# Performance work log

Measured on AMD Instinct MI355X. Metric: run time of the kernel, lower is better.

The kernel has to match this reference:

```python
import jax, jax.numpy as jnp
import numpy as np

MARGIN = 0.5
AP_VALUE = 0.8
AN_VALUE = 0.4
ABS_W = 1.0


def setup_inputs() -> dict:
    key = jax.random.key(0)
    k1, k2 = jax.random.split(key)
    bs, d = 16384, 64
    inputs = jax.random.normal(k1, (bs, d), dtype=jnp.float32)
    target = jax.random.randint(k2, (bs,), 0, 64, dtype=jnp.int64)
    return {"inputs": inputs, "target": target}


def reference(inputs, target):
    # L2-normalize features (normalize_feature=True)
    x = inputs / jnp.linalg.norm(inputs, axis=-1, keepdims=True)

    # cross-entropy on normalized features treated as logits
    logp = jax.nn.log_softmax(x, axis=-1)  # [bs, d]
    loss_ce = -jnp.mean(jnp.take_along_axis(logp, target[:, None], axis=1))

    # cosine-similarity matrix [bs, bs]
    dist = x @ x.T

    is_pos = target[None, :] == target[:, None]
    # hard mining: min similarity among positives, max among negatives (per row)
    dist_ap = jnp.min(jnp.where(is_pos, dist, jnp.inf), axis=1)   # [bs]
    dist_an = jnp.max(jnp.where(is_pos, -jnp.inf, dist), axis=1)  # [bs]

    loss = jnp.mean(jax.nn.relu(MARGIN + dist_ap - dist_an))

    # absolute (angular margin) terms
    abs_ap = jax.nn.relu(AP_VALUE - dist_ap)
    abs_an = jax.nn.relu(dist_an - AN_VALUE)
    loss = (jnp.mean(abs_an) + jnp.mean(abs_ap)) * ABS_W + loss

    return loss + loss_ce
```

## Files before the change

### kernel.cpp

```cpp
#include <hip/hip_runtime.h>


#define N_ROWS 16384
#define N_DIM 64

typedef __attribute__((ext_vector_type(8))) short bf16x8;
typedef __attribute__((ext_vector_type(4))) float f32x4;

__device__ inline unsigned short f2bf(float f) {
  unsigned u = __float_as_uint(f);
  unsigned r = u + 0x7fffu + ((u >> 16) & 1u);
  return (unsigned short)(r >> 16);
}

__device__ inline unsigned enc_key(float f) {
  unsigned u = __float_as_uint(f);
  return (u & 0x80000000u) ? ~u : (u | 0x80000000u);
}
__device__ inline float dec_key(unsigned k) {
  unsigned u = (k & 0x80000000u) ? (k ^ 0x80000000u) : ~k;
  return __uint_as_float(u);
}

__device__ inline void g2lds16(const void* g, void* l) {
  __builtin_amdgcn_global_load_lds(
      (const __attribute__((address_space(1))) void*)g,
      (__attribute__((address_space(3))) void*)l, 16, 0, 0);
}

__global__ void prep_kernel(const float* __restrict__ x, const int* __restrict__ tgt,
                            unsigned short* __restrict__ xb, float* __restrict__ ce_row,
                            unsigned* __restrict__ mp_key, unsigned* __restrict__ mn_key,
                            float* __restrict__ out) {
  const int row  = blockIdx.x * 4 + (threadIdx.x >> 6);
  const int lane = threadIdx.x & 63;
  float v  = x[row * N_DIM + lane];
  float ss = v * v;
#pragma unroll
  for (int s = 1; s < 64; s <<= 1) ss += __shfl_xor(ss, s, 64);
  float xn = v * rsqrtf(ss);
  xb[row * N_DIM + lane] = f2bf(xn);

  float mx = xn;
#pragma unroll
  for (int s = 1; s < 64; s <<= 1) mx = fmaxf(mx, __shfl_xor(mx, s, 64));
  float e  = __expf(xn - mx);
  float se = e;
#pragma unroll
  for (int s = 1; s < 64; s <<= 1) se += __shfl_xor(se, s, 64);
  float lse = mx + __logf(se);
  int   t   = tgt[row];
  float xt  = __shfl(xn, t, 64);
  if (lane == 0) {
    ce_row[row] = lse - xt;
    mp_key[row] = 0xFFFFFFFFu;
    mn_key[row] = 0u;
  }
  if (blockIdx.x == 0 && threadIdx.x == 0) out[0] = 0.f;
}

__global__ __launch_bounds__(256, 8)
void mine_kernel(const unsigned short* __restrict__ xb, const int* __restrict__ tgt,
                 unsigned* __restrict__ mp_key, unsigned* __restrict__ mn_key) {
  __shared__ unsigned short Bt[2][4][1024];
  __shared__ unsigned short tjl[N_ROWS / 16];

  const int lane    = threadIdx.x & 63;
  const int wv      = threadIdx.x >> 6;
  const int iblk    = blockIdx.x >> 4;
  const int jspl    = blockIdx.x & 15;
  const int rowbase = iblk * 128 + wv * 32;
  const int m = lane & 15, q = lane >> 4;
  const int jbase = jspl * (N_ROWS / 16);

  bf16x8 a[2][2];
#pragma unroll
  for (int tr = 0; tr < 2; ++tr) {
    const unsigned short* p = xb + (rowbase + tr * 16 + m) * N_DIM + q * 8;
    a[tr][0] = *(const bf16x8*)(p);
    a[tr][1] = *(const bf16x8*)(p + 32);
  }
  int ti[2][4];
#pragma unroll
  for (int tr = 0; tr < 2; ++tr)
#pragma unroll
    for (int r = 0; r < 4; ++r)
      ti[tr][r] = tgt[rowbase + tr * 16 + q * 4 + r];

  float mp[8], mn[8];
#pragma unroll
  for (int k = 0; k < 8; ++k) { mp[k] = __builtin_inff(); mn[k] = -__builtin_inff(); }

  for (int k = threadIdx.x; k < N_ROWS / 16; k += 256)
    tjl[k] = (unsigned short)tgt[jbase + k];

  const unsigned short* src0 =
      xb + (jbase + (lane >> 3)) * N_DIM + (((lane & 7) ^ ((lane >> 3) & 7)) * 8);

#define STAGE(P, BUF)                                                            \
  do {                                                                           \
    const unsigned short* s_ = src0 + ((P) * 64 + wv * 16) * N_DIM;              \
    g2lds16(s_,             (unsigned short*)&Bt[(BUF)][wv][0] + lane * 8);      \
    g2lds16(s_ + 8 * N_DIM, (unsigned short*)&Bt[(BUF)][wv][0] + 512 + lane * 8);\
  } while (0)

  STAGE(0, 0);
  STAGE(1, 1);
  __syncthreads();

  const int roff0 = m * 128 + ((q * 16) ^ ((m & 7) << 4));
  const int roff1 = m * 128 + (((64) + q * 16) ^ ((m & 7) << 4));

  for (int ph = 0; ph < 16; ++ph) {
    const int pb = ph & 1;
#pragma unroll 1
    for (int j4 = 0; j4 < 4; ++j4) {
      const int jc = ph * 4 + j4;
      const char* bb = (const char*)&Bt[pb][j4][0];
      const bf16x8 cb0 = *(const bf16x8*)(bb + roff0);
      const bf16x8 cb1 = *(const bf16x8*)(bb + roff1);
      const int    ctj = tjl[jc * 16 + m];

#pragma unroll
      for (int tr = 0; tr < 2; ++tr) {
        f32x4 acc = {0.f, 0.f, 0.f, 0.f};
        acc = __builtin_amdgcn_mfma_f32_16x16x32_bf16(a[tr][0], cb0, acc, 0, 0, 0);
        acc = __builtin_amdgcn_mfma_f32_16x16x32_bf16(a[tr][1], cb1, acc, 0, 0, 0);
#pragma unroll
        for (int r = 0; r < 4; ++r) {
          const bool  pos = (ctj == ti[tr][r]);
          const float d   = acc[r];
          const int   k   = tr * 4 + r;
          mp[k] = fminf(mp[k], pos ? d : __builtin_inff());
          mn[k] = fmaxf(mn[k], pos ? -__builtin_inff() : d);
        }
      }
    }
    __builtin_amdgcn_s_barrier();
    if (ph < 14) {
      STAGE(ph + 2, pb);
      asm volatile("s_waitcnt vmcnt(2)" ::: "memory");
      __builtin_amdgcn_sched_barrier(0);
      __builtin_amdgcn_s_barrier();
    } else if (ph == 14) {
      asm volatile("s_waitcnt vmcnt(0)" ::: "memory");
      __builtin_amdgcn_sched_barrier(0);
      __builtin_amdgcn_s_barrier();
    }
  }

#pragma unroll
  for (int s = 1; s < 16; s <<= 1) {
#pragma unroll
    for (int k = 0; k < 8; ++k) {
      mp[k] = fminf(mp[k], __shfl_xor(mp[k], s, 64));
      mn[k] = fmaxf(mn[k], __shfl_xor(mn[k], s, 64));
    }
  }
  if (m == 0) {
#pragma unroll
    for (int tr = 0; tr < 2; ++tr)
#pragma unroll
      for (int r = 0; r < 4; ++r) {
        const int row = rowbase + tr * 16 + q * 4 + r;
        atomicMin(&mp_key[row], enc_key(mp[tr * 4 + r]));
        atomicMax(&mn_key[row], enc_key(mn[tr * 4 + r]));
      }
  }
#undef STAGE
}

__global__ void finalize_kernel(const unsigned* __restrict__ mp_key, const unsigned* __restrict__ mn_key,
                                const float* __restrict__ ce_row, float* __restrict__ out) {
  __shared__ float red[16];
  float s = 0.f;
#pragma unroll
  for (int it = 0; it < 2; ++it) {
    const int r = it * 8192 + blockIdx.x * 1024 + threadIdx.x;
    float ap = dec_key(mp_key[r]);
    float an = dec_key(mn_key[r]);
    s += fmaxf(0.5f + ap - an, 0.f) + fmaxf(0.8f - ap, 0.f) +
         fmaxf(an - 0.4f, 0.f) + ce_row[r];
  }
#pragma unroll
  for (int sh = 1; sh < 64; sh <<= 1) s += __shfl_xor(s, sh, 64);
  const int wv = threadIdx.x >> 6;
  if ((threadIdx.x & 63) == 0) red[wv] = s;
  __syncthreads();
  if (threadIdx.x == 0) {
    float t = 0.f;
#pragma unroll
    for (int w = 0; w < 16; ++w) t += red[w];
    atomicAdd(out, t * (1.0f / N_ROWS));
  }
}

extern "C" void kernel_launch(void* const* d_in, const int* in_sizes, int n_in,
                              void* d_out, int out_size, void* d_ws, size_t ws_size,
                              hipStream_t stream) {
  const float* x   = (const float*)d_in[0];
  const int*   tgt = (const int*)d_in[1];
  char* ws = (char*)d_ws;

  unsigned short* xb     = (unsigned short*)ws;
  unsigned*       mp_key = (unsigned*)(ws + (2u << 20));
  unsigned*       mn_key = (unsigned*)(ws + (2u << 20) + (64u << 10));
  float*          ce_row = (float*)(ws + (2u << 20) + (128u << 10));
  float*          out    = (float*)d_out;

  prep_kernel<<<N_ROWS / 4, 256, 0, stream>>>(x, tgt, xb, ce_row, mp_key, mn_key, out);
  mine_kernel<<<(N_ROWS / 128) * 16, 256, 0, stream>>>(xb, tgt, mp_key, mn_key);
  finalize_kernel<<<8, 1024, 0, stream>>>(mp_key, mn_key, ce_row, out);
}
```

Measured before the change: 157.3 us.

## Software-pipeline MFMA and mining across column tiles, simplify LDS staging

Unrolls the per-phase column-tile loop and software-pipelines it so the MFMAs for the next 16-column tile are issued before the min/max mining of the previous tile's results, overlapping matrix-core latency with VALU work. LDS staging moves from a prefetch-two-ahead scheme with explicit vmcnt waits and double barriers to a prefetch-one-ahead issue at the top of each phase followed by a single __syncthreads. Launch bounds drop from 8 to 6 waves per SIMD to leave room for the extra live accumulators. The shallower prefetch and lower occupancy may expose more load latency.

Measured after the change: 199.6 us. 1.27x slower.

```diff
diff --git a/kernel.cpp b/kernel.cpp
--- a/kernel.cpp
+++ b/kernel.cpp
@@ -59,7 +59,7 @@
   if (blockIdx.x == 0 && threadIdx.x == 0) out[0] = 0.f;
 }
 
-__global__ __launch_bounds__(256, 8)
+__global__ __launch_bounds__(256, 6)
 void mine_kernel(const unsigned short* __restrict__ xb, const int* __restrict__ tgt,
                  unsigned* __restrict__ mp_key, unsigned* __restrict__ mn_key) {
   __shared__ unsigned short Bt[2][4][1024];
@@ -97,57 +97,74 @@
   const unsigned short* src0 =
       xb + (jbase + (lane >> 3)) * N_DIM + (((lane & 7) ^ ((lane >> 3) & 7)) * 8);
 
-#define STAGE(P, BUF)                                                            \
-  do {                                                                           \
-    const unsigned short* s_ = src0 + ((P) * 64 + wv * 16) * N_DIM;              \
+#define STAGE(P_, BUF)                                                           \
+  do {                                                                           \
+    const unsigned short* s_ = src0 + ((P_) * 64 + wv * 16) * N_DIM;             \
     g2lds16(s_,             (unsigned short*)&Bt[(BUF)][wv][0] + lane * 8);      \
     g2lds16(s_ + 8 * N_DIM, (unsigned short*)&Bt[(BUF)][wv][0] + 512 + lane * 8);\
   } while (0)
 
   STAGE(0, 0);
-  STAGE(1, 1);
   __syncthreads();
 
   const int roff0 = m * 128 + ((q * 16) ^ ((m & 7) << 4));
   const int roff1 = m * 128 + (((64) + q * 16) ^ ((m & 7) << 4));
 
+#define MFMA_JC(D0, D1, CB0, CB1)                                                \
+  do {                                                                           \
+    const f32x4 z_ = {0.f, 0.f, 0.f, 0.f};                                       \
+    D0 = __builtin_amdgcn_mfma_f32_16x16x32_bf16(a[0][0], CB0, z_, 0, 0, 0);     \
+    D0 = __builtin_amdgcn_mfma_f32_16x16x32_bf16(a[0][1], CB1, D0, 0, 0, 0);     \
+    D1 = __builtin_amdgcn_mfma_f32_16x16x32_bf16(a[1][0], CB0, z_, 0, 0, 0);     \
+    D1 = __builtin_amdgcn_mfma_f32_16x16x32_bf16(a[1][1], CB1, D1, 0, 0, 0);     \
+  } while (0)
+
+#define JC_STEP(J4, D0, D1, CTV)                                                 \
+  do {                                                                           \
+    const bf16x8 cb0_ = *(const bf16x8*)(bb + (J4) * 2048 + roff0);              \
+    const bf16x8 cb1_ = *(const bf16x8*)(bb + (J4) * 2048 + roff1);              \
+    CTV = (int)tjl[(ph * 4 + (J4)) * 16 + m];                                    \
+    MFMA_JC(D0, D1, cb0_, cb1_);                                                 \
+  } while (0)
+
+#define MINE(A0, A1, CT)                                                         \
+  do {                                                                           \
+    _Pragma("unroll")                                                            \
+    for (int r = 0; r < 4; ++r) {                                                \
+      const bool p0 = ((CT) == ti[0][r]);                                        \
+      mp[r] = fminf(mp[r], p0 ? (A0)[r] : __builtin_inff());                     \
+      mn[r] = fmaxf(mn[r], p0 ? -__builtin_inff() : (A0)[r]);                    \
+      const bool p1 = ((CT) == ti[1][r]);                                        \
+      mp[4 + r] = fminf(mp[4 + r], p1 ? (A1)[r] : __builtin_inff());             \
+      mn[4 + r] = fmaxf(mn[4 + r], p1 ? -__builtin_inff() : (A1)[r]);            \
+    }                                                                            \
+  } while (0)
+
+  f32x4 pA0, pA1, qB0, qB1;
+  int pctj = 0, c0, c1, c2;
+
+#pragma unroll 1
   for (int ph = 0; ph < 16; ++ph) {
     const int pb = ph & 1;
-#pragma unroll 1
-    for (int j4 = 0; j4 < 4; ++j4) {
-      const int jc = ph * 4 + j4;
-      const char* bb = (const char*)&Bt[pb][j4][0];
-      const bf16x8 cb0 = *(const bf16x8*)(bb + roff0);
-      const bf16x8 cb1 = *(const bf16x8*)(bb + roff1);
-      const int    ctj = tjl[jc * 16 + m];
-
-#pragma unroll
-      for (int tr = 0; tr < 2; ++tr) {
-        f32x4 acc = {0.f, 0.f, 0.f, 0.f};
-        acc = __builtin_amdgcn_mfma_f32_16x16x32_bf16(a[tr][0], cb0, acc, 0, 0, 0);
-        acc = __builtin_amdgcn_mfma_f32_16x16x32_bf16(a[tr][1], cb1, acc, 0, 0, 0);
-#pragma unroll
-        for (int r = 0; r < 4; ++r) {
-          const bool  pos = (ctj == ti[tr][r]);
-          const float d   = acc[r];
-          const int   k   = tr * 4 + r;
-          mp[k] = fminf(mp[k], pos ? d : __builtin_inff());
-          mn[k] = fmaxf(mn[k], pos ? -__builtin_inff() : d);
-        }
-      }
-    }
-    __builtin_amdgcn_s_barrier();
-    if (ph < 14) {
-      STAGE(ph + 2, pb);
-      asm volatile("s_waitcnt vmcnt(2)" ::: "memory");
-      __builtin_amdgcn_sched_barrier(0);
-      __builtin_amdgcn_s_barrier();
-    } else if (ph == 14) {
-      asm volatile("s_waitcnt vmcnt(0)" ::: "memory");
-      __builtin_amdgcn_sched_barrier(0);
-      __builtin_amdgcn_s_barrier();
-    }
-  }
+    if (ph < 15) STAGE(ph + 1, pb ^ 1);
+    const char* bb = (const char*)&Bt[pb][0][0];
+
+    JC_STEP(0, qB0, qB1, c0);
+    if (ph) MINE(pA0, pA1, pctj);
+    JC_STEP(1, pA0, pA1, c1);
+    MINE(qB0, qB1, c0);
+    JC_STEP(2, qB0, qB1, c2);
+    MINE(pA0, pA1, c1);
+    JC_STEP(3, pA0, pA1, pctj);
+    MINE(qB0, qB1, c2);
+
+    __syncthreads();
+  }
+  MINE(pA0, pA1, pctj);
+#undef MINE
+#undef JC_STEP
+#undef MFMA_JC
+#undef STAGE
 
 #pragma unroll
   for (int s = 1; s < 16; s <<= 1) {
@@ -167,7 +184,6 @@
         atomicMax(&mn_key[row], enc_key(mn[tr * 4 + r]));
       }
   }
-#undef STAGE
 }
 
 __global__ void finalize_kernel(const unsigned* __restrict__ mp_key, const unsigned* __restrict__ mn_key,
```

## Simplify LDS prefetch pipeline, hand-write MFMA asm, drop softmax max-subtraction

Applied to the files above, without the earlier changes.

The mining kernel's two-deep LDS prefetch, with its split barriers and manual vmcnt waits, becomes a one-phase-ahead prefetch issued at the top of each phase, followed by a single __syncthreads. The two MFMAs per tile are now inline asm with hand-placed s_nop padding, to cover the accumulator hazard without relying on the compiler. The prep kernel drops the max reduction before exp, which is safe because the inputs are L2-normalised to [-1, 1]. The explicit nops and the opaque asm may serialise MFMA issue and stop the compiler from interleaving the two row tiles.

Result: slower. 162.9 us (+3.6%).

```diff
diff --git a/kernel.cpp b/kernel.cpp
--- a/kernel.cpp
+++ b/kernel.cpp
@@ -41,14 +41,11 @@
   float xn = v * rsqrtf(ss);
   xb[row * N_DIM + lane] = f2bf(xn);
 
-  float mx = xn;
-#pragma unroll
-  for (int s = 1; s < 64; s <<= 1) mx = fmaxf(mx, __shfl_xor(mx, s, 64));
-  float e  = __expf(xn - mx);
+  float e  = __expf(xn);
   float se = e;
 #pragma unroll
   for (int s = 1; s < 64; s <<= 1) se += __shfl_xor(se, s, 64);
-  float lse = mx + __logf(se);
+  float lse = __logf(se);
   int   t   = tgt[row];
   float xt  = __shfl(xn, t, 64);
   if (lane == 0) {
@@ -97,15 +94,14 @@
   const unsigned short* src0 =
       xb + (jbase + (lane >> 3)) * N_DIM + (((lane & 7) ^ ((lane >> 3) & 7)) * 8);
 
-#define STAGE(P, BUF)                                                            \
+#define STAGE(P_, BUF)                                                           \
   do {                                                                           \
-    const unsigned short* s_ = src0 + ((P) * 64 + wv * 16) * N_DIM;              \
+    const unsigned short* s_ = src0 + ((P_) * 64 + wv * 16) * N_DIM;             \
     g2lds16(s_,             (unsigned short*)&Bt[(BUF)][wv][0] + lane * 8);      \
     g2lds16(s_ + 8 * N_DIM, (unsigned short*)&Bt[(BUF)][wv][0] + 512 + lane * 8);\
   } while (0)
 
   STAGE(0, 0);
-  STAGE(1, 1);
   __syncthreads();
 
   const int roff0 = m * 128 + ((q * 16) ^ ((m & 7) << 4));
@@ -113,6 +109,7 @@
 
   for (int ph = 0; ph < 16; ++ph) {
     const int pb = ph & 1;
+    if (ph < 15) STAGE(ph + 1, pb ^ 1);
 #pragma unroll 1
     for (int j4 = 0; j4 < 4; ++j4) {
       const int jc = ph * 4 + j4;
@@ -124,8 +121,12 @@
 #pragma unroll
       for (int tr = 0; tr < 2; ++tr) {
         f32x4 acc = {0.f, 0.f, 0.f, 0.f};
-        acc = __builtin_amdgcn_mfma_f32_16x16x32_bf16(a[tr][0], cb0, acc, 0, 0, 0);
-        acc = __builtin_amdgcn_mfma_f32_16x16x32_bf16(a[tr][1], cb1, acc, 0, 0, 0);
+        asm("s_nop 1\n\t"
+            "v_mfma_f32_16x16x32_bf16 %0, %1, %2, %0"
+            : "+v"(acc) : "v"(a[tr][0]), "v"(cb0));
+        asm("v_mfma_f32_16x16x32_bf16 %0, %1, %2, %0\n\t"
+            "s_nop 7\n\ts_nop 2"
+            : "+v"(acc) : "v"(a[tr][1]), "v"(cb1));
 #pragma unroll
         for (int r = 0; r < 4; ++r) {
           const bool  pos = (ctj == ti[tr][r]);
@@ -136,18 +137,9 @@
         }
       }
     }
-    __builtin_amdgcn_s_barrier();
-    if (ph < 14) {
-      STAGE(ph + 2, pb);
-      asm volatile("s_waitcnt vmcnt(2)" ::: "memory");
-      __builtin_amdgcn_sched_barrier(0);
-      __builtin_amdgcn_s_barrier();
-    } else if (ph == 14) {
-      asm volatile("s_waitcnt vmcnt(0)" ::: "memory");
-      __builtin_amdgcn_sched_barrier(0);
-      __builtin_amdgcn_s_barrier();
-    }
-  }
+    __syncthreads();
+  }
+#undef STAGE
 
 #pragma unroll
   for (int s = 1; s < 16; s <<= 1) {
@@ -167,7 +159,6 @@
         atomicMax(&mn_key[row], enc_key(mn[tr * 4 + r]));
       }
   }
-#undef STAGE
 }
 
 __global__ void finalize_kernel(const unsigned* __restrict__ mp_key, const unsigned* __restrict__ mn_key,
```
